# Performance work log

Measured on AMD Instinct MI355X. Metric: run time of the kernel, lower is better.

Reference implementation:

```python
import jax, jax.numpy as jnp
import numpy as np

N_NODES = 50000


def setup_inputs() -> dict:
    key = jax.random.key(0)
    ks = jax.random.split(key, 10)
    E = 800000
    x = jax.random.normal(ks[0], (N_NODES, 256), dtype=jnp.float32)
    src = jax.random.randint(ks[1], (E,), 0, N_NODES, dtype=jnp.int32)
    dst = jax.random.randint(ks[2], (E,), 0, N_NODES, dtype=jnp.int32)
    w = jax.random.uniform(ks[3], (E,), dtype=jnp.float32)
    W1 = jax.random.normal(ks[4], (256, 128), dtype=jnp.float32) / np.sqrt(256)
    b1 = jnp.zeros((128,), dtype=jnp.float32)
    W2 = jax.random.normal(ks[5], (128, 128), dtype=jnp.float32) / np.sqrt(128)
    b2 = jnp.zeros((128,), dtype=jnp.float32)
    W3 = jax.random.normal(ks[6], (128, 64), dtype=jnp.float32) / np.sqrt(128)
    b3 = jnp.zeros((64,), dtype=jnp.float32)
    return {"x": x, "src": src, "dst": dst, "w": w,
            "W1": W1, "b1": b1, "W2": W2, "b2": b2, "W3": W3, "b3": b3}


def _graph_conv(x, src, dst, w, W, b):
    # dense projection then edge-weighted gather-multiply-scatter-sum
    h = x @ W + b                              # [N, d_out]
    msgs = h[src] * w[:, None]                 # [E, d_out] per-edge messages
    return jax.ops.segment_sum(msgs, dst, num_segments=N_NODES)


def reference(x, src, dst, w, W1, b1, W2, b2, W3, b3):
    h = _graph_conv(x, src, dst, w, W1, b1)
    h = jax.nn.relu(h)
    h = _graph_conv(h, src, dst, w, W2, b2)
    h = jax.nn.relu(h)
    h = _graph_conv(h, src, dst, w, W3, b3)
    return h
```

## Files before the change

### kernel.cpp

```cpp
#include <hip/hip_runtime.h>
#include <hip/hip_bf16.h>

#define N_NODES 50000
#define BSHIFT  6
#define BSIZE   64
#define NBUCK   ((N_NODES + BSIZE - 1) / BSIZE)
#define BIN_BLOCKS 256

using short8  = __attribute__((ext_vector_type(8))) short;
using short4v = __attribute__((ext_vector_type(4))) short;
using floatx4 = __attribute__((ext_vector_type(4))) float;

__device__ inline short f32_to_bf16_bits(float f) {
    __hip_bfloat16 h = __float2bfloat16(f);
    return *reinterpret_cast<short*>(&h);
}

template<int K, int N, bool A_F32>
__global__ __launch_bounds__(256) void mfma_gemm(const void* __restrict__ Araw,
                                                 const short* __restrict__ WTf,
                                                 const float* __restrict__ bias,
                                                 short* __restrict__ C, int M)
{
    constexpr int KS = K / 32;
    constexpr int CT = N / 32;
    constexpr int LK = K + 8;

    __shared__ __align__(16) short As[64][LK];

    const int tid  = threadIdx.x;
    const int wave = tid >> 6;
    const int lane = tid & 63;
    const int l15  = lane & 15;
    const int lk   = (lane >> 4) * 8;
    const int wr   = wave >> 1;
    const int wc   = wave & 1;
    const int r0   = blockIdx.x * 64;

    if (A_F32) {
        const float* Af = (const float*)Araw;
#pragma unroll
        for (int it = 0; it < 64 * (K / 4) / 256; ++it) {
            const int idx = it * 256 + tid;
            const int row = idx / (K / 4);
            const int c4  = idx % (K / 4);
            const int gr  = min(r0 + row, M - 1);
            const float4 v = *reinterpret_cast<const float4*>(&Af[(size_t)gr * K + c4 * 4]);
            short4v s;
            s[0] = f32_to_bf16_bits(v.x); s[1] = f32_to_bf16_bits(v.y);
            s[2] = f32_to_bf16_bits(v.z); s[3] = f32_to_bf16_bits(v.w);
            *reinterpret_cast<short4v*>(&As[row][c4 * 4]) = s;
        }
    } else {
        const short* Ab = (const short*)Araw;
#pragma unroll
        for (int it = 0; it < 64 * (K / 8) / 256; ++it) {
            const int idx = it * 256 + tid;
            const int row = idx / (K / 8);
            const int c8  = idx % (K / 8);
            const int gr  = min(r0 + row, M - 1);
            const short8 v = *reinterpret_cast<const short8*>(&Ab[(size_t)gr * K + c8 * 8]);
            *reinterpret_cast<short8*>(&As[row][c8 * 8]) = v;
        }
    }
    __syncthreads();

    float bv[CT];
#pragma unroll
    for (int t = 0; t < CT; ++t) bv[t] = bias[wc * (N / 2) + t * 16 + l15];

    floatx4 acc[2][CT];
#pragma unroll
    for (int rt = 0; rt < 2; ++rt)
#pragma unroll
        for (int t = 0; t < CT; ++t) acc[rt][t] = (floatx4){0.f, 0.f, 0.f, 0.f};

#pragma unroll
    for (int ks = 0; ks < KS; ++ks) {
        short8 b[CT];
#pragma unroll
        for (int t = 0; t < CT; ++t) {
            const int tg = wc * CT + t;
            b[t] = *reinterpret_cast<const short8*>(&WTf[((size_t)(tg * KS + ks) * 64 + lane) * 8]);
        }
        short8 a[2];
#pragma unroll
        for (int rt = 0; rt < 2; ++rt)
            a[rt] = *reinterpret_cast<const short8*>(&As[wr * 32 + rt * 16 + l15][ks * 32 + lk]);
#pragma unroll
        for (int rt = 0; rt < 2; ++rt)
#pragma unroll
            for (int t = 0; t < CT; ++t)
                acc[rt][t] = __builtin_amdgcn_mfma_f32_16x16x32_bf16(a[rt], b[t], acc[rt][t], 0, 0, 0);
    }

    const int rowg = (lane >> 4) * 4;
#pragma unroll
    for (int rt = 0; rt < 2; ++rt)
#pragma unroll
        for (int t = 0; t < CT; ++t)
#pragma unroll
            for (int j = 0; j < 4; ++j) {
                const int gr = r0 + wr * 32 + rt * 16 + rowg + j;
                if (gr < M)
                    C[(size_t)gr * N + wc * (N / 2) + t * 16 + l15] =
                        f32_to_bf16_bits(acc[rt][t][j] + bv[t]);
            }
}

__device__ inline void wt_frag(const float* __restrict__ W, short* __restrict__ out,
                               int K, int N, int u)
{
    const int lane = u & 63;
    const int rest = u >> 6;
    const int KS   = K >> 5;
    const int ks   = rest % KS;
    const int tg   = rest / KS;
    const int n    = tg * 16 + (lane & 15);
    const int kb   = ks * 32 + (lane >> 4) * 8;
    short8 s;
#pragma unroll
    for (int e = 0; e < 8; ++e) s[e] = f32_to_bf16_bits(W[(size_t)(kb + e) * N + n]);
    *reinterpret_cast<short8*>(&out[(size_t)u * 8]) = s;
}

__global__ __launch_bounds__(256) void wt_all(const float* __restrict__ W1, short* __restrict__ WT1,
                                              const float* __restrict__ W2, short* __restrict__ WT2,
                                              const float* __restrict__ W3, short* __restrict__ WT3)
{
    const int u = blockIdx.x * 256 + threadIdx.x;
    if (u < 4096)             wt_frag(W1, WT1, 256, 128, u);
    else if (u < 4096 + 2048) wt_frag(W2, WT2, 128, 128, u - 4096);
    else if (u < 7168)        wt_frag(W3, WT3, 128, 64,  u - 6144);
}


__global__ __launch_bounds__(256) void bin_hist(const int* __restrict__ dst,
                                                int* __restrict__ hist_g, int E)
{
    __shared__ int hist[NBUCK];
    for (int t = threadIdx.x; t < NBUCK; t += 256) hist[t] = 0;
    __syncthreads();
    const int chunk = (E + BIN_BLOCKS - 1) / BIN_BLOCKS;
    const int beg = blockIdx.x * chunk;
    const int end = min(beg + chunk, E);
    for (int i = beg + threadIdx.x; i < end; i += 256)
        atomicAdd(&hist[dst[i] >> BSHIFT], 1);
    __syncthreads();
    for (int t = threadIdx.x; t < NBUCK; t += 256)
        hist_g[blockIdx.x * NBUCK + t] = hist[t];
}

__global__ __launch_bounds__(256) void bin_scan_blocks(const int* __restrict__ hist_g,
                                                       int* __restrict__ blockbase,
                                                       int* __restrict__ tot)
{
    __shared__ int s[BIN_BLOCKS];
    const int b = blockIdx.x;
    const int t = threadIdx.x;
    const int v = hist_g[t * NBUCK + b];
    s[t] = v;
    __syncthreads();
#pragma unroll
    for (int off = 1; off < BIN_BLOCKS; off <<= 1) {
        const int tmp = (t >= off) ? s[t - off] : 0;
        __syncthreads();
        s[t] += tmp;
        __syncthreads();
    }
    blockbase[t * NBUCK + b] = s[t] - v;
    if (t == BIN_BLOCKS - 1) tot[b] = s[t];
}

__global__ __launch_bounds__(256) void bin_scan_tot(const int* __restrict__ tot,
                                                    int* __restrict__ bucket_base)
{
    __shared__ int psum[256];
    const int t = threadIdx.x;
    int vals[4];
    int s = 0;
#pragma unroll
    for (int j = 0; j < 4; ++j) {
        const int idx = t * 4 + j;
        vals[j] = (idx < NBUCK) ? tot[idx] : 0;
        s += vals[j];
    }
    psum[t] = s;
    __syncthreads();
#pragma unroll
    for (int off = 1; off < 256; off <<= 1) {
        const int tmp = (t >= off) ? psum[t - off] : 0;
        __syncthreads();
        psum[t] += tmp;
        __syncthreads();
    }
    int run = psum[t] - s;
#pragma unroll
    for (int j = 0; j < 4; ++j) {
        const int idx = t * 4 + j;
        if (idx < NBUCK) bucket_base[idx] = run;
        run += vals[j];
    }
    if (t == 255) bucket_base[NBUCK] = run;
}

__global__ __launch_bounds__(256) void bin_write(const int* __restrict__ src,
                                                 const int* __restrict__ dst,
                                                 const float* __restrict__ w,
                                                 const int* __restrict__ blockbase,
                                                 const int* __restrict__ bucket_base,
                                                 int2* __restrict__ tmp, int E)
{
    __shared__ int cur[NBUCK];
    for (int t = threadIdx.x; t < NBUCK; t += 256)
        cur[t] = bucket_base[t] + blockbase[blockIdx.x * NBUCK + t];
    __syncthreads();
    const int chunk = (E + BIN_BLOCKS - 1) / BIN_BLOCKS;
    const int beg = blockIdx.x * chunk;
    const int end = min(beg + chunk, E);
    for (int i = beg + threadIdx.x; i < end; i += 256) {
        const int d = dst[i];
        const int pos = atomicAdd(&cur[d >> BSHIFT], 1);
        tmp[pos] = make_int2((src[i] << BSHIFT) | (d & (BSIZE - 1)), __float_as_int(w[i]));
    }
}

__global__ __launch_bounds__(256) void fine_fill2(const int2* __restrict__ tmp,
                                                  const int* __restrict__ bucket_base,
                                                  unsigned int* __restrict__ csr_ew,
                                                  int* __restrict__ row_ptr)
{
    __shared__ int hist[BSIZE];
    __shared__ int basel[BSIZE];
    const int b    = blockIdx.x;
    const int t    = threadIdx.x;
    const int rbeg = bucket_base[b];
    const int rend = bucket_base[b + 1];

    if (t < BSIZE) hist[t] = 0;
    __syncthreads();
    for (int i = rbeg + t; i < rend; i += 256)
        atomicAdd(&hist[((unsigned)tmp[i].x) & (BSIZE - 1)], 1);
    __syncthreads();

    if (t < BSIZE) {
        const int v = hist[t];
        int inc = v;
#pragma unroll
        for (int off = 1; off < BSIZE; off <<= 1) {
            const int u = __shfl_up(inc, off, 64);
            if (t >= off) inc += u;
        }
        const int excl = rbeg + inc - v;
        basel[t] = excl;
        const int node = (b << BSHIFT) + t;
        if (node < N_NODES) row_ptr[node] = excl;
        if (b == NBUCK - 1 && t == 0) row_ptr[N_NODES] = bucket_base[NBUCK];
    }
    __syncthreads();

    for (int i = rbeg + t; i < rend; i += 256) {
        const int2 e = tmp[i];
        const unsigned ex = (unsigned)e.x;
        const int pos = atomicAdd(&basel[ex & (BSIZE - 1)], 1);
        const unsigned wb = (unsigned short)f32_to_bf16_bits(__int_as_float(e.y));
        csr_ew[pos] = ((ex >> BSHIFT) << 16) | wb;
    }
}

template<bool RELU>
__global__ __launch_bounds__(256) void pull128_bf(const unsigned int* __restrict__ h,
                                                  const int* __restrict__ row_ptr,
                                                  const unsigned int* __restrict__ csr_ew,
                                                  unsigned int* __restrict__ out, int n_nodes)
{
    const int wave = threadIdx.x >> 6;
    const int lane = threadIdx.x & 63;
    const int node = blockIdx.x * 4 + wave;
    if (node >= n_nodes) return;

    const int beg = row_ptr[node];
    const int end = row_ptr[node + 1];

    float ax[8], ay[8];
#pragma unroll
    for (int u = 0; u < 8; ++u) { ax[u] = 0.f; ay[u] = 0.f; }

    for (int c = beg; c < end; c += 64) {
        const int idx = c + lane;
        const unsigned ew = (idx < end) ? csr_ew[idx] : 0u;
        const int cnt = min(64, end - c);

        for (int j = 0; j < cnt; j += 8) {
            unsigned e[8];
#pragma unroll
            for (int u = 0; u < 8; ++u) {
                const unsigned v = __shfl(ew, j + u);
                e[u] = (j + u < cnt) ? v : 0u;
            }
            unsigned p[8];
#pragma unroll
            for (int u = 0; u < 8; ++u)
                p[u] = h[(size_t)(e[u] >> 16) * 64 + lane];
#pragma unroll
            for (int u = 0; u < 8; ++u) {
                const float wv = __int_as_float(e[u] << 16);
                ax[u] = fmaf(__int_as_float(p[u] << 16), wv, ax[u]);
                ay[u] = fmaf(__int_as_float(p[u] & 0xffff0000u), wv, ay[u]);
            }
        }
    }

    float axs = ((ax[0] + ax[1]) + (ax[2] + ax[3])) + ((ax[4] + ax[5]) + (ax[6] + ax[7]));
    float ays = ((ay[0] + ay[1]) + (ay[2] + ay[3])) + ((ay[4] + ay[5]) + (ay[6] + ay[7]));
    if (RELU) { axs = fmaxf(axs, 0.f); ays = fmaxf(ays, 0.f); }
    const unsigned lo = (unsigned short)f32_to_bf16_bits(axs);
    const unsigned hi = (unsigned short)f32_to_bf16_bits(ays);
    out[(size_t)node * 64 + lane] = lo | (hi << 16);
}

__global__ __launch_bounds__(256) void pull64_bf(const unsigned int* __restrict__ h,
                                                 const int* __restrict__ row_ptr,
                                                 const unsigned int* __restrict__ csr_ew,
                                                 float2* __restrict__ out, int n_nodes)
{
    const int wave = threadIdx.x >> 6;
    const int lane = threadIdx.x & 63;
    const int half = lane >> 5;
    const int l32  = lane & 31;
    const int node = blockIdx.x * 8 + wave * 2 + half;
    if (node >= n_nodes) return;

    const int beg = row_ptr[node];
    const int end = row_ptr[node + 1];

    float ax[8], ay[8];
#pragma unroll
    for (int u = 0; u < 8; ++u) { ax[u] = 0.f; ay[u] = 0.f; }

    for (int c = beg; c < end; c += 32) {
        const int idx = c + l32;
        const unsigned ew = (idx < end) ? csr_ew[idx] : 0u;
        const int cnt = min(32, end - c);

        for (int j = 0; j < cnt; j += 8) {
            unsigned e[8];
#pragma unroll
            for (int u = 0; u < 8; ++u) {
                const unsigned v = __shfl(ew, j + u, 32);
                e[u] = (j + u < cnt) ? v : 0u;
            }
            unsigned p[8];
#pragma unroll
            for (int u = 0; u < 8; ++u)
                p[u] = h[(size_t)(e[u] >> 16) * 32 + l32];
#pragma unroll
            for (int u = 0; u < 8; ++u) {
                const float wv = __int_as_float(e[u] << 16);
                ax[u] = fmaf(__int_as_float(p[u] << 16), wv, ax[u]);
                ay[u] = fmaf(__int_as_float(p[u] & 0xffff0000u), wv, ay[u]);
            }
        }
    }

    const float axs = ((ax[0] + ax[1]) + (ax[2] + ax[3])) + ((ax[4] + ax[5]) + (ax[6] + ax[7]));
    const float ays = ((ay[0] + ay[1]) + (ay[2] + ay[3])) + ((ay[4] + ay[5]) + (ay[6] + ay[7]));
    out[(size_t)node * 32 + l32] = make_float2(axs, ays);
}

extern "C" void kernel_launch(void* const* d_in, const int* in_sizes, int n_in,
                              void* d_out, int out_size, void* d_ws, size_t ws_size,
                              hipStream_t stream)
{
    const float* x   = (const float*)d_in[0];
    const int*   src = (const int*)  d_in[1];
    const int*   dst = (const int*)  d_in[2];
    const float* w   = (const float*)d_in[3];
    const float* W1  = (const float*)d_in[4];
    const float* b1  = (const float*)d_in[5];
    const float* W2  = (const float*)d_in[6];
    const float* b2  = (const float*)d_in[7];
    const float* W3  = (const float*)d_in[8];
    const float* b3  = (const float*)d_in[9];

    const int E = in_sizes[1];
    const int M = N_NODES;

    short* hA  = (short*)d_ws;
    short* hB  = hA + (size_t)M * 128;
    short* WT1 = hB + (size_t)M * 128;
    short* WT2 = WT1 + 128 * 256;
    short* WT3 = WT2 + 128 * 128;
    unsigned int* csr_ew = (unsigned int*)(WT3 + 64 * 128);
    int2*  tmp_ew      = (int2*)(csr_ew + ((E + 1) & ~1));
    int*   row_ptr     = (int*)(tmp_ew + E);
    int*   hist_g      = row_ptr + 50048;
    int*   blockbase   = hist_g + 200704;
    int*   bucket_base = blockbase + 200704;
    int*   tot         = bucket_base + 1024;

    const int gemm_blocks = (M + 63) / 64;

    wt_all<<<28, 256, 0, stream>>>(W1, WT1, W2, WT2, W3, WT3);
    bin_hist<<<BIN_BLOCKS, 256, 0, stream>>>(dst, hist_g, E);
    bin_scan_blocks<<<NBUCK, BIN_BLOCKS, 0, stream>>>(hist_g, blockbase, tot);
    bin_scan_tot<<<1, 256, 0, stream>>>(tot, bucket_base);
    bin_write<<<BIN_BLOCKS, 256, 0, stream>>>(src, dst, w, blockbase, bucket_base, tmp_ew, E);
    fine_fill2<<<NBUCK, 256, 0, stream>>>(tmp_ew, bucket_base, csr_ew, row_ptr);

    mfma_gemm<256, 128, true><<<gemm_blocks, 256, 0, stream>>>(x, WT1, b1, hA, M);
    pull128_bf<true><<<(M + 3) / 4, 256, 0, stream>>>((const unsigned int*)hA, row_ptr, csr_ew,
                                                      (unsigned int*)hB, M);
    mfma_gemm<128, 128, false><<<gemm_blocks, 256, 0, stream>>>(hB, WT2, b2, hA, M);
    pull128_bf<true><<<(M + 3) / 4, 256, 0, stream>>>((const unsigned int*)hA, row_ptr, csr_ew,
                                                      (unsigned int*)hB, M);
    mfma_gemm<128, 64, false><<<gemm_blocks, 256, 0, stream>>>(hB, WT3, b3, hA, M);
    pull64_bf<<<(M + 7) / 8, 256, 0, stream>>>((const unsigned int*)hA, row_ptr, csr_ew,
                                               (float2*)d_out, M);
}
```

Baseline: 153.3 us.

## Fuse pull aggregation with following GEMM and merge histogram with weight prep

```diff
diff --git a/kernel.cpp b/kernel.cpp
--- a/kernel.cpp
+++ b/kernel.cpp
@@ -108,6 +108,121 @@
             }
 }
 
+template<int K, int N>
+__global__ __launch_bounds__(512) void fused_pull_gemm(const unsigned int* __restrict__ h,
+                                                       const int* __restrict__ row_ptr,
+                                                       const unsigned int* __restrict__ csr_ew,
+                                                       const short* __restrict__ WTf,
+                                                       const float* __restrict__ bias,
+                                                       short* __restrict__ C, int M)
+{
+    static_assert(K == 128, "pull input dim is 128");
+    constexpr int KS   = K / 32;
+    constexpr int LK   = K + 8;
+    constexpr int COLT = 2;
+    constexpr int WCG  = N / (COLT * 16);
+    constexpr int WRG  = 8 / WCG;
+    constexpr int ROWT = 64 / (WRG * 16);
+
+    __shared__ __align__(16) short As[64][LK];
+
+    const int tid  = threadIdx.x;
+    const int wave = tid >> 6;
+    const int lane = tid & 63;
+    const int r0   = blockIdx.x * 64;
+
+    for (int i = 0; i < 8; ++i) {
+        const int lrow = wave * 8 + i;
+        const int node = r0 + lrow;
+        if (node < M) {
+            const int beg = row_ptr[node];
+            const int end = row_ptr[node + 1];
+
+            float ax[8], ay[8];
+#pragma unroll
+            for (int u = 0; u < 8; ++u) { ax[u] = 0.f; ay[u] = 0.f; }
+
+            for (int c = beg; c < end; c += 64) {
+                const int idx = c + lane;
+                const unsigned ew = (idx < end) ? csr_ew[idx] : 0u;
+                const int cnt = min(64, end - c);
+                for (int j = 0; j < cnt; j += 8) {
+                    unsigned e[8];
+#pragma unroll
+                    for (int u = 0; u < 8; ++u) {
+                        const unsigned v = __shfl(ew, j + u);
+                        e[u] = (j + u < cnt) ? v : 0u;
+                    }
+                    unsigned p[8];
+#pragma unroll
+                    for (int u = 0; u < 8; ++u)
+                        p[u] = h[(size_t)(e[u] >> 16) * 64 + lane];
+#pragma unroll
+                    for (int u = 0; u < 8; ++u) {
+                        const float wv = __int_as_float(e[u] << 16);
+                        ax[u] = fmaf(__int_as_float(p[u] << 16), wv, ax[u]);
+                        ay[u] = fmaf(__int_as_float(p[u] & 0xffff0000u), wv, ay[u]);
+                    }
+                }
+            }
+            float axs = ((ax[0] + ax[1]) + (ax[2] + ax[3])) + ((ax[4] + ax[5]) + (ax[6] + ax[7]));
+            float ays = ((ay[0] + ay[1]) + (ay[2] + ay[3])) + ((ay[4] + ay[5]) + (ay[6] + ay[7]));
+            axs = fmaxf(axs, 0.f); ays = fmaxf(ays, 0.f);
+            const unsigned lo = (unsigned short)f32_to_bf16_bits(axs);
+            const unsigned hi = (unsigned short)f32_to_bf16_bits(ays);
+            *reinterpret_cast<unsigned int*>(&As[lrow][2 * lane]) = lo | (hi << 16);
+        }
+    }
+    __syncthreads();
+
+    const int l15 = lane & 15;
+    const int lk  = (lane >> 4) * 8;
+    const int wr  = wave / WCG;
+    const int wc  = wave % WCG;
+
+    float bv[COLT];
+#pragma unroll
+    for (int t = 0; t < COLT; ++t) bv[t] = bias[wc * COLT * 16 + t * 16 + l15];
+
+    floatx4 acc[ROWT][COLT];
+#pragma unroll
+    for (int rt = 0; rt < ROWT; ++rt)
+#pragma unroll
+        for (int t = 0; t < COLT; ++t) acc[rt][t] = (floatx4){0.f, 0.f, 0.f, 0.f};
+
+#pragma unroll
+    for (int ks = 0; ks < KS; ++ks) {
+        short8 b[COLT];
+#pragma unroll
+        for (int t = 0; t < COLT; ++t) {
+            const int tg = wc * COLT + t;
+            b[t] = *reinterpret_cast<const short8*>(&WTf[((size_t)(tg * KS + ks) * 64 + lane) * 8]);
+        }
+        short8 a[ROWT];
+#pragma unroll
+        for (int rt = 0; rt < ROWT; ++rt)
+            a[rt] = *reinterpret_cast<const short8*>(&As[wr * (ROWT * 16) + rt * 16 + l15][ks * 32 + lk]);
+#pragma unroll
+        for (int rt = 0; rt < ROWT; ++rt)
+#pragma unroll
+            for (int t = 0; t < COLT; ++t)
+                acc[rt][t] = __builtin_amdgcn_mfma_f32_16x16x32_bf16(a[rt], b[t], acc[rt][t], 0, 0, 0);
+    }
+
+    const int rowg = (lane >> 4) * 4;
+#pragma unroll
+    for (int rt = 0; rt < ROWT; ++rt)
+#pragma unroll
+        for (int t = 0; t < COLT; ++t)
+#pragma unroll
+            for (int j = 0; j < 4; ++j) {
+                const int gr = r0 + wr * (ROWT * 16) + rt * 16 + rowg + j;
+                if (gr < M)
+                    C[(size_t)gr * N + wc * COLT * 16 + t * 16 + l15] =
+                        f32_to_bf16_bits(acc[rt][t][j] + bv[t]);
+            }
+}
+
 __device__ inline void wt_frag(const float* __restrict__ W, short* __restrict__ out,
                                int K, int N, int u)
 {
@@ -124,31 +239,30 @@
     *reinterpret_cast<short8*>(&out[(size_t)u * 8]) = s;
 }
 
-__global__ __launch_bounds__(256) void wt_all(const float* __restrict__ W1, short* __restrict__ WT1,
-                                              const float* __restrict__ W2, short* __restrict__ WT2,
-                                              const float* __restrict__ W3, short* __restrict__ WT3)
-{
-    const int u = blockIdx.x * 256 + threadIdx.x;
-    if (u < 4096)             wt_frag(W1, WT1, 256, 128, u);
-    else if (u < 4096 + 2048) wt_frag(W2, WT2, 128, 128, u - 4096);
-    else if (u < 7168)        wt_frag(W3, WT3, 128, 64,  u - 6144);
-}
-
-
-__global__ __launch_bounds__(256) void bin_hist(const int* __restrict__ dst,
-                                                int* __restrict__ hist_g, int E)
-{
-    __shared__ int hist[NBUCK];
-    for (int t = threadIdx.x; t < NBUCK; t += 256) hist[t] = 0;
-    __syncthreads();
-    const int chunk = (E + BIN_BLOCKS - 1) / BIN_BLOCKS;
-    const int beg = blockIdx.x * chunk;
-    const int end = min(beg + chunk, E);
-    for (int i = beg + threadIdx.x; i < end; i += 256)
-        atomicAdd(&hist[dst[i] >> BSHIFT], 1);
-    __syncthreads();
-    for (int t = threadIdx.x; t < NBUCK; t += 256)
-        hist_g[blockIdx.x * NBUCK + t] = hist[t];
+__global__ __launch_bounds__(256) void prep_kernel(const int* __restrict__ dst,
+                                                   int* __restrict__ hist_g, int E,
+                                                   const float* __restrict__ W1, short* __restrict__ WT1,
+                                                   const float* __restrict__ W2, short* __restrict__ WT2,
+                                                   const float* __restrict__ W3, short* __restrict__ WT3)
+{
+    if (blockIdx.x < BIN_BLOCKS) {
+        __shared__ int hist[NBUCK];
+        for (int t = threadIdx.x; t < NBUCK; t += 256) hist[t] = 0;
+        __syncthreads();
+        const int chunk = (E + BIN_BLOCKS - 1) / BIN_BLOCKS;
+        const int beg = blockIdx.x * chunk;
+        const int end = min(beg + chunk, E);
+        for (int i = beg + threadIdx.x; i < end; i += 256)
+            atomicAdd(&hist[dst[i] >> BSHIFT], 1);
+        __syncthreads();
+        for (int t = threadIdx.x; t < NBUCK; t += 256)
+            hist_g[blockIdx.x * NBUCK + t] = hist[t];
+    } else {
+        const int u = (blockIdx.x - BIN_BLOCKS) * 256 + threadIdx.x;
+        if (u < 4096)             wt_frag(W1, WT1, 256, 128, u);
+        else if (u < 4096 + 2048) wt_frag(W2, WT2, 128, 128, u - 4096);
+        else if (u < 7168)        wt_frag(W3, WT3, 128, 64,  u - 6144);
+    }
 }
 
 __global__ __launch_bounds__(256) void bin_scan_blocks(const int* __restrict__ hist_g,
@@ -268,57 +382,6 @@
     }
 }
 
-template<bool RELU>
-__global__ __launch_bounds__(256) void pull128_bf(const unsigned int* __restrict__ h,
-                                                  const int* __restrict__ row_ptr,
-                                                  const unsigned int* __restrict__ csr_ew,
-                                                  unsigned int* __restrict__ out, int n_nodes)
-{
-    const int wave = threadIdx.x >> 6;
-    const int lane = threadIdx.x & 63;
-    const int node = blockIdx.x * 4 + wave;
-    if (node >= n_nodes) return;
-
-    const int beg = row_ptr[node];
-    const int end = row_ptr[node + 1];
-
-    float ax[8], ay[8];
-#pragma unroll
-    for (int u = 0; u < 8; ++u) { ax[u] = 0.f; ay[u] = 0.f; }
-
-    for (int c = beg; c < end; c += 64) {
-        const int idx = c + lane;
-        const unsigned ew = (idx < end) ? csr_ew[idx] : 0u;
-        const int cnt = min(64, end - c);
-
-        for (int j = 0; j < cnt; j += 8) {
-            unsigned e[8];
-#pragma unroll
-            for (int u = 0; u < 8; ++u) {
-                const unsigned v = __shfl(ew, j + u);
-                e[u] = (j + u < cnt) ? v : 0u;
-            }
-            unsigned p[8];
-#pragma unroll
-            for (int u = 0; u < 8; ++u)
-                p[u] = h[(size_t)(e[u] >> 16) * 64 + lane];
-#pragma unroll
-            for (int u = 0; u < 8; ++u) {
-                const float wv = __int_as_float(e[u] << 16);
-                ax[u] = fmaf(__int_as_float(p[u] << 16), wv, ax[u]);
-                ay[u] = fmaf(__int_as_float(p[u] & 0xffff0000u), wv, ay[u]);
-            }
-        }
-    }
-
-    float axs = ((ax[0] + ax[1]) + (ax[2] + ax[3])) + ((ax[4] + ax[5]) + (ax[6] + ax[7]));
-    float ays = ((ay[0] + ay[1]) + (ay[2] + ay[3])) + ((ay[4] + ay[5]) + (ay[6] + ay[7]));
-    if (RELU) { axs = fmaxf(axs, 0.f); ays = fmaxf(ays, 0.f); }
-    const unsigned lo = (unsigned short)f32_to_bf16_bits(axs);
-    const unsigned hi = (unsigned short)f32_to_bf16_bits(ays);
-    out[(size_t)node * 64 + lane] = lo | (hi << 16);
-}
-
 __global__ __launch_bounds__(256) void pull64_bf(const unsigned int* __restrict__ h,
                                                  const int* __restrict__ row_ptr,
                                                  const unsigned int* __restrict__ csr_ew,
@@ -342,7 +405,6 @@
         const int idx = c + l32;
         const unsigned ew = (idx < end) ? csr_ew[idx] : 0u;
         const int cnt = min(32, end - c);
-
         for (int j = 0; j < cnt; j += 8) {
             unsigned e[8];
 #pragma unroll
@@ -399,22 +461,18 @@
     int*   bucket_base = blockbase + 200704;
     int*   tot         = bucket_base + 1024;
 
-    const int gemm_blocks = (M + 63) / 64;
-
-    wt_all<<<28, 256, 0, stream>>>(W1, WT1, W2, WT2, W3, WT3);
-    bin_hist<<<BIN_BLOCKS, 256, 0, stream>>>(dst, hist_g, E);
+    prep_kernel<<<BIN_BLOCKS + 28, 256, 0, stream>>>(dst, hist_g, E, W1, WT1, W2, WT2, W3, WT3);
     bin_scan_blocks<<<NBUCK, BIN_BLOCKS, 0, stream>>>(hist_g, blockbase, tot);
     bin_scan_tot<<<1, 256, 0, stream>>>(tot, bucket_base);
     bin_write<<<BIN_BLOCKS, 256, 0, stream>>>(src, dst, w, blockbase, bucket_base, tmp_ew, E);
     fine_fill2<<<NBUCK, 256, 0, stream>>>(tmp_ew, bucket_base, csr_ew, row_ptr);
 
-    mfma_gemm<256, 128, true><<<gemm_blocks, 256, 0, stream>>>(x, WT1, b1, hA, M);
-    pull128_bf<true><<<(M + 3) / 4, 256, 0, stream>>>((const unsigned int*)hA, row_ptr, csr_ew,
-                                                      (unsigned int*)hB, M);
-    mfma_gemm<128, 128, false><<<gemm_blocks, 256, 0, stream>>>(hB, WT2, b2, hA, M);
-    pull128_bf<true><<<(M + 3) / 4, 256, 0, stream>>>((const unsigned int*)hA, row_ptr, csr_ew,
-                                                      (unsigned int*)hB, M);
-    mfma_gemm<128, 64, false><<<gemm_blocks, 256, 0, stream>>>(hB, WT3, b3, hA, M);
+    mfma_gemm<256, 128, true><<<NBUCK, 256, 0, stream>>>(x, WT1, b1, hA, M);
+
+    fused_pull_gemm<128, 128><<<NBUCK, 512, 0, stream>>>((const unsigned int*)hA, row_ptr, csr_ew,
+                                                         WT2, b2, hB, M);
+    fused_pull_gemm<128, 64><<<NBUCK, 512, 0, stream>>>((const unsigned int*)hB, row_ptr, csr_ew,
+                                                        WT3, b3, hA, M);
     pull64_bf<<<(M + 7) / 8, 256, 0, stream>>>((const unsigned int*)hA, row_ptr, csr_ew,
                                                (float2*)d_out, M);
 }
```

New measurement: 147.6 us. 1.04x faster.
